# Kernel tuning notes

Hardware: AMD Instinct MI355X
Metric: run time of the kernel (lower is better)

Reference implementation:

```python
import jax, jax.numpy as jnp
import numpy as np

THRESHOLD = 8.0
BN_EPS = 1e-5


def setup_inputs() -> dict:
    key = jax.random.key(0)
    k1, k2 = jax.random.split(key)
    B, C, H, W = 2, 128, 64, 64
    x = jax.random.normal(k1, (B, C, H, W), dtype=jnp.float32)
    W_fc = jax.random.normal(k2, (C, C), dtype=jnp.float32) * (1.0 / np.sqrt(C))
    b_fc = jnp.zeros((C,), dtype=jnp.float32)
    gamma = jnp.ones((C,), dtype=jnp.float32)
    beta = jnp.zeros((C,), dtype=jnp.float32)
    return {"x": x, "W_fc": W_fc, "b_fc": b_fc, "gamma": gamma, "beta": beta}


def _mean_agg(X, path):
    # X: [B,N,C], path: [B,N,N] (col->row). out = rownorm(path) @ X
    out = jnp.matmul(path, X)
    s = jnp.sum(path, axis=2, keepdims=True)  # [B,N,1]
    norm = jnp.where(s > 0, 1.0 / s, 0.0)     # inf -> 0 as in torch code
    return norm * out


def reference(x, W_fc, b_fc, gamma, beta):
    b, c, h, w = x.shape
    N = h * w
    # [B,N,C] token features
    xf = jnp.transpose(x.reshape(b, c, N), (0, 2, 1))
    # pairwise euclidean distance (cdist, p=2)
    sq = jnp.sum(xf * xf, axis=-1)  # [B,N]
    d2 = sq[:, :, None] + sq[:, None, :] - 2.0 * jnp.einsum('bnc,bmc->bnm', xf, xf)
    dist = jnp.sqrt(jnp.maximum(d2, 0.0))
    Hg = (dist < THRESHOLD).astype(xf.dtype)  # [B,N,N] hypergraph incidence
    # HyperGraphConv: y = fc(x); E = mean(H^T @ y); out = mean(H @ E); res = y + out
    y = jnp.einsum('bnc,dc->bnd', xf, W_fc) + b_fc
    E = _mean_agg(y, jnp.swapaxes(Hg, 1, 2))
    x_out = _mean_agg(E, Hg)
    xe = y + x_out  # [B,N,C]
    # back to [B,C,H,W]
    xo = jnp.transpose(xe, (0, 2, 1)).reshape(b, c, h, w)
    # BatchNorm2d (training mode: batch stats over B,H,W) + SiLU
    mean = jnp.mean(xo, axis=(0, 2, 3), keepdims=True)
    var = jnp.var(xo, axis=(0, 2, 3), keepdims=True)
    xn = (xo - mean) * jax.lax.rsqrt(var + BN_EPS)
    xn = gamma[None, :, None, None] * xn + beta[None, :, None, None]
    return xn * jax.nn.sigmoid(xn)
```

## Files before the change

kernel.cpp:

```cpp
#include <hip/hip_runtime.h>

typedef unsigned short ushort_t;
typedef unsigned int   uint32;
typedef unsigned long long u64;
typedef __bf16 bf16_t;
typedef bf16_t bf16x8 __attribute__((ext_vector_type(8)));
typedef float  f32x4  __attribute__((ext_vector_type(4)));

#define N_TOK 4096
#define C_DIM 128
#define NTOT  8192
#define THRESH2 64.0f

#define XF_OFF  (0u)
#define YF_OFF  (2u<<20)
#define EF_OFF  (6u<<20)
#define XE_OFF  (10u<<20)
#define SQ_OFF  (14u<<20)
#define BN_OFF  ((14u<<20) + 32768u)
#define HB_OFF  (16u<<20)
#define WS_NEED ((size_t)(24u<<20))

__device__ __forceinline__ float b2f(ushort_t u){ return __uint_as_float(((uint32)u)<<16); }
__device__ __forceinline__ ushort_t f2b(float f){
    uint32 u = __float_as_uint(f);
    u += 0x7fffu + ((u>>16)&1u);
    return (ushort_t)(u>>16);
}
__device__ __forceinline__ u64 shfl_u64(u64 v, int src){
    uint32 lo = (uint32)v, hi = (uint32)(v>>32);
    lo = __shfl(lo, src); hi = __shfl(hi, src);
    return ((u64)hi<<32)|lo;
}
__device__ __forceinline__ u64 shfl_xor_u64(u64 v, int m){
    uint32 lo = (uint32)v, hi = (uint32)(v>>32);
    lo = __shfl_xor(lo, m); hi = __shfl_xor(hi, m);
    return ((u64)hi<<32)|lo;
}

__global__ __launch_bounds__(256) void k_fc(const float* __restrict__ x,
                                            const float* __restrict__ W,
                                            const float* __restrict__ bfc,
                                            ushort_t* __restrict__ Xf,
                                            float* __restrict__ Yf,
                                            float* __restrict__ sq,
                                            float* __restrict__ bn){
    __shared__ ushort_t Xs[64*136];
    __shared__ ushort_t Ws[128*136];
    int tid = threadIdx.x;
    int t0 = blockIdx.x * 64;
    int b  = t0 >> 12;
    int n0 = t0 & 4095;
    if (blockIdx.x == 0) bn[tid] = 0.f;
    const float* xb = x + (size_t)b * C_DIM * N_TOK + n0;
    #pragma unroll
    for (int k=0;k<8;k++){
        int idx = tid + 256*k;
        int c = idx >> 4, n4 = (idx & 15)*4;
        float4 v = *(const float4*)(xb + (size_t)c*N_TOK + n4);
        Xs[(n4+0)*136 + c] = f2b(v.x);
        Xs[(n4+1)*136 + c] = f2b(v.y);
        Xs[(n4+2)*136 + c] = f2b(v.z);
        Xs[(n4+3)*136 + c] = f2b(v.w);
    }
    #pragma unroll
    for (int k=0;k<16;k++){
        int idx = tid + 256*k;
        int d = idx >> 5, c4 = (idx & 31)*4;
        float4 v = *(const float4*)(W + d*C_DIM + c4);
        uint2 u;
        u.x = (uint32)f2b(v.x) | ((uint32)f2b(v.y)<<16);
        u.y = (uint32)f2b(v.z) | ((uint32)f2b(v.w)<<16);
        *(uint2*)(&Ws[d*136 + c4]) = u;
    }
    __syncthreads();
    #pragma unroll
    for (int k=0;k<4;k++){
        int idx = tid + 256*k;
        int row = idx >> 4, c8 = (idx & 15)*8;
        uint4 o = *(const uint4*)(&Xs[row*136 + c8]);
        *(uint4*)(Xf + (size_t)(t0 + row)*C_DIM + c8) = o;
    }
    {
        int tok = tid >> 2, p = tid & 3;
        const ushort_t* xr = &Xs[tok*136 + p*32];
        float sacc = 0.f;
        #pragma unroll
        for (int i=0;i<16;i++){
            uint32 u = *(const uint32*)(&xr[i*2]);
            float v0 = __uint_as_float(u<<16);
            float v1 = __uint_as_float(u & 0xffff0000u);
            sacc = fmaf(v0, v0, sacc);
            sacc = fmaf(v1, v1, sacc);
        }
        sacc += __shfl_xor(sacc, 1);
        sacc += __shfl_xor(sacc, 2);
        if (p == 0) sq[t0 + tok] = sacc;
    }
    int wv = tid >> 6, lane = tid & 63;
    int qd = lane >> 4, m = lane & 15;
    f32x4 acc[8] = {{0,0,0,0},{0,0,0,0},{0,0,0,0},{0,0,0,0},
                    {0,0,0,0},{0,0,0,0},{0,0,0,0},{0,0,0,0}};
    #pragma unroll
    for (int kc=0;kc<4;kc++){
        bf16x8 af = *(const bf16x8*)(&Xs[(wv*16 + m)*136 + kc*32 + qd*8]);
        #pragma unroll
        for (int ct=0;ct<8;ct++){
            bf16x8 bfr = *(const bf16x8*)(&Ws[(ct*16+m)*136 + kc*32 + qd*8]);
            acc[ct] = __builtin_amdgcn_mfma_f32_16x16x32_bf16(af, bfr, acc[ct], 0, 0, 0);
        }
    }
    int row = t0 + wv*16 + qd*4;
    #pragma unroll
    for (int ct=0;ct<8;ct++){
        int d = ct*16 + m;
        float bias = bfc[d];
        #pragma unroll
        for (int r=0;r<4;r++)
            Yf[(size_t)(row + r)*C_DIM + d] = acc[ct][r] + bias;
    }
}

__global__ __launch_bounds__(256) void k_gram(const ushort_t* __restrict__ Xf,
                                              const float* __restrict__ sq,
                                              u64* __restrict__ Hb){
    __shared__ ushort_t Al[128*136];
    __shared__ ushort_t Bl[64*136];
    int tid = threadIdx.x;
    int i0 = blockIdx.x * 128, j0 = blockIdx.y * 64, b = blockIdx.z;
    const ushort_t* XfA = Xf + (size_t)(b*N_TOK + i0)*C_DIM;
    const ushort_t* XfB = Xf + (size_t)(b*N_TOK + j0)*C_DIM;
    #pragma unroll
    for (int k=0;k<8;k++){
        int q = tid + 256*k;
        int row = q >> 4, cp = (q & 15)*8;
        *(uint4*)(&Al[row*136 + cp]) = *(const uint4*)(XfA + row*C_DIM + cp);
    }
    #pragma unroll
    for (int k=0;k<4;k++){
        int q = tid + 256*k;
        int row = q >> 4, cp = (q & 15)*8;
        *(uint4*)(&Bl[row*136 + cp]) = *(const uint4*)(XfB + row*C_DIM + cp);
    }
    __syncthreads();
    int wv = tid >> 6, lane = tid & 63;
    int qd = lane >> 4, m = lane & 15;
    f32x4 acc[2][4] = {{{0,0,0,0},{0,0,0,0},{0,0,0,0},{0,0,0,0}},
                       {{0,0,0,0},{0,0,0,0},{0,0,0,0},{0,0,0,0}}};
    #pragma unroll
    for (int kc=0;kc<4;kc++){
        bf16x8 a0 = *(const bf16x8*)(&Al[(wv*32 +      m)*136 + kc*32 + qd*8]);
        bf16x8 a1 = *(const bf16x8*)(&Al[(wv*32 + 16 + m)*136 + kc*32 + qd*8]);
        #pragma unroll
        for (int ct=0;ct<4;ct++){
            bf16x8 bfr = *(const bf16x8*)(&Bl[(ct*16+m)*136 + kc*32 + qd*8]);
            acc[0][ct] = __builtin_amdgcn_mfma_f32_16x16x32_bf16(a0, bfr, acc[0][ct], 0, 0, 0);
            acc[1][ct] = __builtin_amdgcn_mfma_f32_16x16x32_bf16(a1, bfr, acc[1][ct], 0, 0, 0);
        }
    }
    float sqj[4];
    #pragma unroll
    for (int ct=0;ct<4;ct++) sqj[ct] = sq[b*N_TOK + j0 + ct*16 + m];
    #pragma unroll
    for (int rt=0;rt<2;rt++){
        int ib = i0 + wv*32 + rt*16 + qd*4;
        float sqi[4];
        #pragma unroll
        for (int r=0;r<4;r++) sqi[r] = sq[b*N_TOK + ib + r];
        #pragma unroll
        for (int r=0;r<4;r++){
            u64 bits = 0;
            #pragma unroll
            for (int ct=0;ct<4;ct++){
                float d2 = sqi[r] + sqj[ct] - 2.0f*acc[rt][ct][r];
                if (d2 < THRESH2) bits |= (u64)1 << (ct*16 + m);
            }
            bits |= shfl_xor_u64(bits, 1);
            bits |= shfl_xor_u64(bits, 2);
            bits |= shfl_xor_u64(bits, 4);
            bits |= shfl_xor_u64(bits, 8);
            if (m == 0) Hb[(size_t)(b*N_TOK + ib + r)*64 + blockIdx.y] = bits;
        }
    }
}

template<int MODE>
__global__ __launch_bounds__(256) void k_aggs(const u64* __restrict__ Hb,
                                              const float* __restrict__ V,
                                              const float* __restrict__ Yf,
                                              float* __restrict__ Out){
    int tid = threadIdx.x;
    int wv = tid >> 6, lane = tid & 63;
    int row = blockIdx.x * 4 + wv;
    int b = row >> 12;
    u64 myw = Hb[(size_t)row*64 + lane];
    int cnt = __builtin_popcountll(myw);
    cnt += __shfl_xor(cnt, 1);
    cnt += __shfl_xor(cnt, 2);
    cnt += __shfl_xor(cnt, 4);
    cnt += __shfl_xor(cnt, 8);
    cnt += __shfl_xor(cnt, 16);
    cnt += __shfl_xor(cnt, 32);
    float acc0 = 0.f, acc1 = 0.f;
    const float* Vb = V + (size_t)b*N_TOK*C_DIM;
    u64 nz = __ballot(myw != 0);
    while (nz){
        int wdi = __builtin_ctzll(nz);
        nz &= nz - 1;
        u64 mw = shfl_u64(myw, wdi);
        while (mw){
            int j = wdi*64 + __builtin_ctzll(mw);
            mw &= mw - 1;
            acc0 += Vb[(size_t)j*C_DIM + lane];
            acc1 += Vb[(size_t)j*C_DIM + lane + 64];
        }
    }
    float norm = (cnt > 0) ? (1.0f/(float)cnt) : 0.0f;
    size_t o = (size_t)row*C_DIM;
    if (MODE == 0){
        Out[o + lane]      = acc0*norm;
        Out[o + lane + 64] = acc1*norm;
    } else {
        Out[o + lane]      = Yf[o + lane]      + acc0*norm;
        Out[o + lane + 64] = Yf[o + lane + 64] + acc1*norm;
    }
}

__global__ __launch_bounds__(256) void k_bnstats(const float* __restrict__ Xe,
                                                 float* __restrict__ bn){
    __shared__ float r1[256], r2[256];
    int tid = threadIdx.x;
    int c = tid & 127, h = tid >> 7;
    int tb = blockIdx.x * 64;
    float sm = 0.f, ss = 0.f;
    for (int tt = tb + h; tt < tb + 64; tt += 2){
        float v = Xe[(size_t)tt*C_DIM + c];
        sm += v; ss = fmaf(v, v, ss);
    }
    r1[tid] = sm; r2[tid] = ss;
    __syncthreads();
    if (tid < 128){
        atomicAdd(&bn[c],       r1[tid] + r1[tid+128]);
        atomicAdd(&bn[128 + c], r2[tid] + r2[tid+128]);
    }
}

__global__ __launch_bounds__(256) void k_out(const float* __restrict__ Xe,
                                             const float* __restrict__ bn,
                                             const float* __restrict__ gamma,
                                             const float* __restrict__ beta,
                                             float* __restrict__ out){
    __shared__ float tile[32][33];
    int tx = threadIdx.x, ty = threadIdx.y;
    int n0 = blockIdx.x*32, c0 = blockIdx.y*32, b = blockIdx.z;
    int c = c0 + tx;
    float inv = 1.0f / (float)NTOT;
    float mean = bn[c] * inv;
    float var  = bn[128 + c]*inv - mean*mean;
    float scale = gamma[c] * rsqrtf(var + 1e-5f);
    float shift = beta[c] - mean*scale;
    #pragma unroll
    for (int k=0;k<4;k++){
        int nl = ty + 8*k;
        float v = Xe[(size_t)(b*N_TOK + n0 + nl)*C_DIM + c];
        v = scale*v + shift;
        float sg = 1.0f/(1.0f + __expf(-v));
        tile[tx][nl] = v * sg;
    }
    __syncthreads();
    #pragma unroll
    for (int k=0;k<4;k++){
        int cl = ty + 8*k;
        out[(size_t)(b*C_DIM + c0 + cl)*N_TOK + n0 + tx] = tile[cl][tx];
    }
}

extern "C" void kernel_launch(void* const* d_in, const int* in_sizes, int n_in,
                              void* d_out, int out_size, void* d_ws, size_t ws_size,
                              hipStream_t stream){
    if (ws_size < WS_NEED) return;
    const float* x     = (const float*)d_in[0];
    const float* W     = (const float*)d_in[1];
    const float* bfc   = (const float*)d_in[2];
    const float* gamma = (const float*)d_in[3];
    const float* beta  = (const float*)d_in[4];
    char* ws = (char*)d_ws;
    ushort_t* Xf = (ushort_t*)(ws + XF_OFF);
    float*    Yf = (float*)(ws + YF_OFF);
    float*    Ef = (float*)(ws + EF_OFF);
    float*    Xe = (float*)(ws + XE_OFF);
    float*    sq = (float*)(ws + SQ_OFF);
    float*    bn = (float*)(ws + BN_OFF);
    u64*      Hb = (u64*)(ws + HB_OFF);
    float* out = (float*)d_out;

    k_fc<<<dim3(128), dim3(256), 0, stream>>>(x, W, bfc, Xf, Yf, sq, bn);
    k_gram<<<dim3(32,64,2), dim3(256), 0, stream>>>(Xf, sq, Hb);
    k_aggs<0><<<dim3(2048), dim3(256), 0, stream>>>(Hb, Yf, Yf, Ef);
    k_aggs<1><<<dim3(2048), dim3(256), 0, stream>>>(Hb, Ef, Yf, Xe);
    k_bnstats<<<dim3(128), dim3(256), 0, stream>>>(Xe, bn);
    k_out<<<dim3(128,4,2), dim3(32,8), 0, stream>>>(Xe, bn, gamma, beta, out);
}
```

Measured before the change: 118.7 us.

## Exploit Gram symmetry, fuse BN stats into aggregation, split FC across channels

The Gram/threshold kernel now computes only upper-triangular block tiles (1056 instead of 2048 per batch). It writes the transposed bitmask via a shared-memory bit transpose, so roughly half of the MFMA and staging work is skipped. BatchNorm statistics are accumulated inside the second aggregation kernel into 8 partial buffers, which removes the separate stats kernel and its re-read of Xe; the output kernel sums the partials. The FC kernel is split over two output-channel halves to double its grid. The cost is extra atomics and a triangular index decode per block, and diagonal tiles may write a few words redundantly.

```diff
diff --git a/kernel.cpp b/kernel.cpp
--- a/kernel.cpp
+++ b/kernel.cpp
@@ -44,14 +44,18 @@
                                             ushort_t* __restrict__ Xf,
                                             float* __restrict__ Yf,
                                             float* __restrict__ sq,
-                                            float* __restrict__ bn){
+                                            float* __restrict__ bnp){
     __shared__ ushort_t Xs[64*136];
-    __shared__ ushort_t Ws[128*136];
+    __shared__ ushort_t Ws[64*136];
     int tid = threadIdx.x;
     int t0 = blockIdx.x * 64;
+    int dh = blockIdx.y;
     int b  = t0 >> 12;
     int n0 = t0 & 4095;
-    if (blockIdx.x == 0) bn[tid] = 0.f;
+    if (blockIdx.x == 0 && dh == 0){
+        #pragma unroll
+        for (int k=0;k<8;k++) bnp[tid + 256*k] = 0.f;
+    }
     const float* xb = x + (size_t)b * C_DIM * N_TOK + n0;
     #pragma unroll
     for (int k=0;k<8;k++){
@@ -63,11 +67,12 @@
         Xs[(n4+2)*136 + c] = f2b(v.z);
         Xs[(n4+3)*136 + c] = f2b(v.w);
     }
-    #pragma unroll
-    for (int k=0;k<16;k++){
+    const float* Wb = W + (size_t)dh*64*C_DIM;
+    #pragma unroll
+    for (int k=0;k<8;k++){
         int idx = tid + 256*k;
         int d = idx >> 5, c4 = (idx & 31)*4;
-        float4 v = *(const float4*)(W + d*C_DIM + c4);
+        float4 v = *(const float4*)(Wb + d*C_DIM + c4);
         uint2 u;
         u.x = (uint32)f2b(v.x) | ((uint32)f2b(v.y)<<16);
         u.y = (uint32)f2b(v.z) | ((uint32)f2b(v.w)<<16);
@@ -75,13 +80,13 @@
     }
     __syncthreads();
     #pragma unroll
-    for (int k=0;k<4;k++){
-        int idx = tid + 256*k;
+    for (int k=0;k<2;k++){
+        int idx = tid + 256*(k + 2*dh);
         int row = idx >> 4, c8 = (idx & 15)*8;
         uint4 o = *(const uint4*)(&Xs[row*136 + c8]);
         *(uint4*)(Xf + (size_t)(t0 + row)*C_DIM + c8) = o;
     }
-    {
+    if (dh == 0){
         int tok = tid >> 2, p = tid & 3;
         const ushort_t* xr = &Xs[tok*136 + p*32];
         float sacc = 0.f;
@@ -99,21 +104,20 @@
     }
     int wv = tid >> 6, lane = tid & 63;
     int qd = lane >> 4, m = lane & 15;
-    f32x4 acc[8] = {{0,0,0,0},{0,0,0,0},{0,0,0,0},{0,0,0,0},
-                    {0,0,0,0},{0,0,0,0},{0,0,0,0},{0,0,0,0}};
+    f32x4 acc[4] = {{0,0,0,0},{0,0,0,0},{0,0,0,0},{0,0,0,0}};
     #pragma unroll
     for (int kc=0;kc<4;kc++){
         bf16x8 af = *(const bf16x8*)(&Xs[(wv*16 + m)*136 + kc*32 + qd*8]);
         #pragma unroll
-        for (int ct=0;ct<8;ct++){
+        for (int ct=0;ct<4;ct++){
             bf16x8 bfr = *(const bf16x8*)(&Ws[(ct*16+m)*136 + kc*32 + qd*8]);
             acc[ct] = __builtin_amdgcn_mfma_f32_16x16x32_bf16(af, bfr, acc[ct], 0, 0, 0);
         }
     }
     int row = t0 + wv*16 + qd*4;
     #pragma unroll
-    for (int ct=0;ct<8;ct++){
-        int d = ct*16 + m;
+    for (int ct=0;ct<4;ct++){
+        int d = dh*64 + ct*16 + m;
         float bias = bfc[d];
         #pragma unroll
         for (int r=0;r<4;r++)
@@ -126,8 +130,15 @@
                                               u64* __restrict__ Hb){
     __shared__ ushort_t Al[128*136];
     __shared__ ushort_t Bl[64*136];
+    __shared__ u64 rowW[128];
+    __shared__ u64 part[256];
     int tid = threadIdx.x;
-    int i0 = blockIdx.x * 128, j0 = blockIdx.y * 64, b = blockIdx.z;
+    int L = blockIdx.x, b = blockIdx.y;
+    int bi = (int)((65.0f - sqrtf(4225.0f - 4.0f*(float)L)) * 0.5f);
+    while (bi > 0 && bi*(65-bi) > L) --bi;
+    while ((bi+1)*(65-(bi+1)) <= L) ++bi;
+    int bj = L - bi*(65-bi) + 2*bi;
+    int i0 = bi*128, j0 = bj*64;
     const ushort_t* XfA = Xf + (size_t)(b*N_TOK + i0)*C_DIM;
     const ushort_t* XfB = Xf + (size_t)(b*N_TOK + j0)*C_DIM;
     #pragma unroll
@@ -163,7 +174,8 @@
     for (int ct=0;ct<4;ct++) sqj[ct] = sq[b*N_TOK + j0 + ct*16 + m];
     #pragma unroll
     for (int rt=0;rt<2;rt++){
-        int ib = i0 + wv*32 + rt*16 + qd*4;
+        int lr = wv*32 + rt*16 + qd*4;
+        int ib = i0 + lr;
         float sqi[4];
         #pragma unroll
         for (int r=0;r<4;r++) sqi[r] = sq[b*N_TOK + ib + r];
@@ -179,8 +191,29 @@
             bits |= shfl_xor_u64(bits, 2);
             bits |= shfl_xor_u64(bits, 4);
             bits |= shfl_xor_u64(bits, 8);
-            if (m == 0) Hb[(size_t)(b*N_TOK + ib + r)*64 + blockIdx.y] = bits;
-        }
+            if (m == 0){
+                Hb[(size_t)(b*N_TOK + ib + r)*64 + bj] = bits;
+                rowW[lr + r] = bits;
+            }
+        }
+    }
+    __syncthreads();
+    {
+        int jj = tid & 63, hw = (tid>>6)&1, sub = tid>>7;
+        u64 p = 0;
+        int ibase = hw*64 + sub*32;
+        #pragma unroll 8
+        for (int ii=0; ii<32; ii++){
+            u64 wrd = rowW[ibase + ii];
+            p |= ((wrd >> jj) & 1ull) << (sub*32 + ii);
+        }
+        part[tid] = p;
+    }
+    __syncthreads();
+    if (tid < 128){
+        int jj = tid & 63, hw = tid >> 6;
+        u64 wt = part[tid] | part[tid + 128];
+        Hb[(size_t)(b*N_TOK + j0 + jj)*64 + 2*bi + hw] = wt;
     }
 }
 
@@ -188,7 +221,10 @@
 __global__ __launch_bounds__(256) void k_aggs(const u64* __restrict__ Hb,
                                               const float* __restrict__ V,
                                               const float* __restrict__ Yf,
-                                              float* __restrict__ Out){
+                                              float* __restrict__ Out,
+                                              float* __restrict__ bnp){
+    __shared__ float r1[4][128];
+    __shared__ float r2[4][128];
     int tid = threadIdx.x;
     int wv = tid >> 6, lane = tid & 63;
     int row = blockIdx.x * 4 + wv;
@@ -221,32 +257,27 @@
         Out[o + lane]      = acc0*norm;
         Out[o + lane + 64] = acc1*norm;
     } else {
-        Out[o + lane]      = Yf[o + lane]      + acc0*norm;
-        Out[o + lane + 64] = Yf[o + lane + 64] + acc1*norm;
-    }
-}
-
-__global__ __launch_bounds__(256) void k_bnstats(const float* __restrict__ Xe,
-                                                 float* __restrict__ bn){
-    __shared__ float r1[256], r2[256];
-    int tid = threadIdx.x;
-    int c = tid & 127, h = tid >> 7;
-    int tb = blockIdx.x * 64;
-    float sm = 0.f, ss = 0.f;
-    for (int tt = tb + h; tt < tb + 64; tt += 2){
-        float v = Xe[(size_t)tt*C_DIM + c];
-        sm += v; ss = fmaf(v, v, ss);
-    }
-    r1[tid] = sm; r2[tid] = ss;
-    __syncthreads();
-    if (tid < 128){
-        atomicAdd(&bn[c],       r1[tid] + r1[tid+128]);
-        atomicAdd(&bn[128 + c], r2[tid] + r2[tid+128]);
+        float xe0 = Yf[o + lane]      + acc0*norm;
+        float xe1 = Yf[o + lane + 64] + acc1*norm;
+        Out[o + lane]      = xe0;
+        Out[o + lane + 64] = xe1;
+        r1[wv][lane]      = xe0;
+        r1[wv][lane + 64] = xe1;
+        r2[wv][lane]      = xe0*xe0;
+        r2[wv][lane + 64] = xe1*xe1;
+        __syncthreads();
+        if (tid < 128){
+            float s1 = r1[0][tid]+r1[1][tid]+r1[2][tid]+r1[3][tid];
+            float s2 = r2[0][tid]+r2[1][tid]+r2[2][tid]+r2[3][tid];
+            int prt = blockIdx.x & 7;
+            atomicAdd(&bnp[prt*256 + tid],       s1);
+            atomicAdd(&bnp[prt*256 + 128 + tid], s2);
+        }
     }
 }
 
 __global__ __launch_bounds__(256) void k_out(const float* __restrict__ Xe,
-                                             const float* __restrict__ bn,
+                                             const float* __restrict__ bnp,
                                              const float* __restrict__ gamma,
                                              const float* __restrict__ beta,
                                              float* __restrict__ out){
@@ -254,9 +285,15 @@
     int tx = threadIdx.x, ty = threadIdx.y;
     int n0 = blockIdx.x*32, c0 = blockIdx.y*32, b = blockIdx.z;
     int c = c0 + tx;
+    float s1 = 0.f, s2 = 0.f;
+    #pragma unroll
+    for (int p=0;p<8;p++){
+        s1 += bnp[p*256 + c];
+        s2 += bnp[p*256 + 128 + c];
+    }
     float inv = 1.0f / (float)NTOT;
-    float mean = bn[c] * inv;
-    float var  = bn[128 + c]*inv - mean*mean;
+    float mean = s1 * inv;
+    float var  = s2*inv - mean*mean;
     float scale = gamma[c] * rsqrtf(var + 1e-5f);
     float shift = beta[c] - mean*scale;
     #pragma unroll
@@ -290,14 +327,13 @@
     float*    Ef = (float*)(ws + EF_OFF);
     float*    Xe = (float*)(ws + XE_OFF);
     float*    sq = (float*)(ws + SQ_OFF);
-    float*    bn = (float*)(ws + BN_OFF);
+    float*    bnp= (float*)(ws + BN_OFF);
     u64*      Hb = (u64*)(ws + HB_OFF);
     float* out = (float*)d_out;
 
-    k_fc<<<dim3(128), dim3(256), 0, stream>>>(x, W, bfc, Xf, Yf, sq, bn);
-    k_gram<<<dim3(32,64,2), dim3(256), 0, stream>>>(Xf, sq, Hb);
-    k_aggs<0><<<dim3(2048), dim3(256), 0, stream>>>(Hb, Yf, Yf, Ef);
-    k_aggs<1><<<dim3(2048), dim3(256), 0, stream>>>(Hb, Ef, Yf, Xe);
-    k_bnstats<<<dim3(128), dim3(256), 0, stream>>>(Xe, bn);
-    k_out<<<dim3(128,4,2), dim3(32,8), 0, stream>>>(Xe, bn, gamma, beta, out);
-}
+    k_fc<<<dim3(128,2), dim3(256), 0, stream>>>(x, W, bfc, Xf, Yf, sq, bnp);
+    k_gram<<<dim3(1056,2), dim3(256), 0, stream>>>(Xf, sq, Hb);
+    k_aggs<0><<<dim3(2048), dim3(256), 0, stream>>>(Hb, Yf, Yf, Ef, bnp);
+    k_aggs<1><<<dim3(2048), dim3(256), 0, stream>>>(Hb, Ef, Yf, Xe, bnp);
+    k_out<<<dim3(128,4,2), dim3(32,8), 0, stream>>>(Xe, bnp, gamma, beta, out);
+}
```

Result: faster. 112.5 us (median of 2 runs) (-5.2%).
